# Performance work log

Hardware: AMD Instinct MI355X
Metric: run time of the kernel (lower is better)

The kernel has to match this reference:

```python
import jax, jax.numpy as jnp
import numpy as np

# CSSA config (index=0): H=W=64, strip windows h_spa=64, w_spa=8, heads=4, C=64
B, HW, C, HEADS = 32, 64, 64, 4
HS, WS = 64, 8          # h_spa, w_spa
HD = C // HEADS          # head_dim = 16
WIN = HS * WS            # 512 tokens per window
SCALE = HD ** -0.5


def setup_inputs() -> dict:
    key = jax.random.key(0)
    k1, k2, k3 = jax.random.split(key, 3)
    qkv = jax.random.normal(k1, (3, B, HW * HW, C), dtype=jnp.float32)
    w_conv = jax.random.normal(k2, (C, 1, 3, 3), dtype=jnp.float32) * 0.1
    b_conv = jax.random.normal(k3, (C,), dtype=jnp.float32) * 0.1
    return {"qkv": qkv, "w_conv": w_conv, "b_conv": b_conv}


def _to_img(x):
    # [B, N, C] -> [B, C, H, W]
    return jnp.transpose(x.reshape(B, HW, HW, C), (0, 3, 1, 2))


def _img2window_heads(x):
    img = _to_img(x)
    img = img.reshape(B, C, HW // HS, HS, HW // WS, WS)
    win = jnp.transpose(img, (0, 2, 4, 3, 5, 1)).reshape(-1, WIN, C)
    return jnp.transpose(win.reshape(-1, WIN, HEADS, HD), (0, 2, 1, 3))


def _v_windows(x):
    # [B, N, C] -> [B*nWin, C, h_spa, w_spa] (image-layout windows for conv)
    img = _to_img(x)
    img = img.reshape(B, C, HW // HS, HS, HW // WS, WS)
    return jnp.transpose(img, (0, 2, 4, 1, 3, 5)).reshape(-1, C, HS, WS)


def reference(qkv, w_conv, b_conv):
    q, k, v = qkv[0], qkv[1], qkv[2]
    qh = _img2window_heads(q) * SCALE
    kh = _img2window_heads(k)
    vw = _v_windows(v)                           # [Bw, C, HS, WS]
    # depthwise 3x3 conv LePE
    lepe = jax.lax.conv_general_dilated(
        vw, w_conv, window_strides=(1, 1), padding=((1, 1), (1, 1)),
        feature_group_count=C,
        dimension_numbers=("NCHW", "OIHW", "NCHW")) + b_conv[None, :, None, None]
    Bw = vw.shape[0]
    lepe = jnp.transpose(lepe.reshape(Bw, HEADS, HD, WIN), (0, 1, 3, 2))
    vh = jnp.transpose(vw.reshape(Bw, HEADS, HD, WIN), (0, 1, 3, 2))
    attn = jax.nn.softmax(jnp.einsum("whqd,whkd->whqk", qh, kh), axis=-1)
    x = jnp.einsum("whqk,whkd->whqd", attn, vh) + lepe
    x = jnp.transpose(x, (0, 2, 1, 3)).reshape(Bw, WIN, C)
    # window2spa
    x = x.reshape(B, HW // HS, HW // WS, HS, WS, C)
    x = jnp.transpose(x, (0, 1, 3, 2, 4, 5)).reshape(B, HW * HW, C)
    return x
```

## Files before the change

kernel.cpp:

```cpp
#include <hip/hip_runtime.h>
#include <stdint.h>

#define KSTR 36
#define VSTR 516

typedef __attribute__((ext_vector_type(4))) short          short4v;
typedef __attribute__((ext_vector_type(4))) float          f32x4;
typedef __attribute__((ext_vector_type(4))) unsigned short us4;
typedef __bf16 bf2_t __attribute__((ext_vector_type(2)));

__device__ __forceinline__ float bf2f(unsigned short u) {
    union { unsigned int i; float f; } x; x.i = ((unsigned int)u) << 16; return x.f;
}
__device__ __forceinline__ unsigned int pk2bf(float lo, float hi) {
#if __has_builtin(__builtin_amdgcn_cvt_pk_bf16_f32)
    union { bf2_t v; unsigned int u; } c;
    c.v = __builtin_amdgcn_cvt_pk_bf16_f32(lo, hi);
    return c.u;
#else
    union { float f; unsigned int u; } a, b; a.f = lo; b.f = hi;
    return __builtin_amdgcn_perm(b.u + 0x8000u, a.u + 0x8000u, 0x07060302u);
#endif
}
__device__ __forceinline__ short4v pk4bf(float a, float b, float c, float d) {
    union { short4v s; unsigned int u[2]; } p;
    p.u[0] = pk2bf(a, b);
    p.u[1] = pk2bf(c, d);
    return p.s;
}

__global__ __launch_bounds__(1024, 4)
void CSSA_69355131896243_kernel(const float* __restrict__ qkv,
                                const float* __restrict__ wconv,
                                const float* __restrict__ bconv,
                                float* __restrict__ out)
{
    __shared__ unsigned short Kl[512 * KSTR];
    __shared__ unsigned short Vt[32 * VSTR];
    __shared__ float Wl[288];
    __shared__ float Bl[32];

    const int tid  = threadIdx.x;
    const int wave = tid >> 6, lane = tid & 63, quad = lane >> 4, l15 = lane & 15;

    const int bid = blockIdx.x;
    const int p   = (bid >> 3) & 1;
    const int win = (bid & 7) * 32 + (bid >> 4);
    const int b   = win >> 3, wx = win & 7;
    const int pc  = p * 32;

    const size_t ONE  = (size_t)32 * 4096 * 64;
    const size_t base = ((size_t)b * 4096 + (size_t)wx * 8) * 64;
    const float* gQ = qkv + base;
    const float* gK = qkv + ONE + base;
    const float* gV = qkv + 2 * ONE + base;

    {
        const int c8 = tid & 7;
        const int t0 = tid >> 3;
        #pragma unroll
        for (int r = 0; r < 4; ++r) {
            const int t = r * 128 + t0;
            const size_t goff = (size_t)(t >> 3) * 4096 + (size_t)(t & 7) * 64 + pc + c8 * 4;
            f32x4 kd = *(const f32x4*)(gK + goff);
            f32x4 vd = *(const f32x4*)(gV + goff);
            union { us4 v; unsigned int u[2]; } kb;
            kb.u[0] = pk2bf(kd[0], kd[1]);
            kb.u[1] = pk2bf(kd[2], kd[3]);
            *(us4*)(&Kl[t * KSTR + c8 * 4]) = kb.v;
            const unsigned int v01 = pk2bf(vd[0], vd[1]);
            const unsigned int v23 = pk2bf(vd[2], vd[3]);
            Vt[(c8 * 4 + 0) * VSTR + t] = (unsigned short)(v01 & 0xffffu);
            Vt[(c8 * 4 + 1) * VSTR + t] = (unsigned short)(v01 >> 16);
            Vt[(c8 * 4 + 2) * VSTR + t] = (unsigned short)(v23 & 0xffffu);
            Vt[(c8 * 4 + 3) * VSTR + t] = (unsigned short)(v23 >> 16);
        }
    }
    if (tid < 288) Wl[tid] = wconv[p * 288 + tid];
    if (tid < 32)  Bl[tid] = bconv[pc + tid];

    const float SCL = 0.25f * 1.44269504088896341f;
    const int hl  = (wave & 1) * 16;
    const int hg  = pc + hl;
    const int q0  = (wave >> 1) * 64;
    short4v qf[4];
    #pragma unroll
    for (int t = 0; t < 4; ++t) {
        const int q = q0 + t * 16 + l15;
        f32x4 qv = *(const f32x4*)(gQ + (size_t)(q >> 3) * 4096 + (size_t)(q & 7) * 64 + hg + quad * 4);
        qf[t] = pk4bf(qv[0] * SCL, qv[1] * SCL, qv[2] * SCL, qv[3] * SCL);
    }
    __syncthreads();

    f32x4 acc[4];
    float lp[4];
    #pragma unroll
    for (int t = 0; t < 4; ++t) { acc[t] = (f32x4)0.0f; lp[t] = 0.0f; }

    #pragma unroll 4
    for (int c = 0; c < 32; ++c) {
        const short4v kf = *(const short4v*)(&Kl[(c * 16 + l15) * KSTR + hl + quad * 4]);
        const short4v vf = *(const short4v*)(&Vt[(hl + l15) * VSTR + c * 16 + quad * 4]);
        #pragma unroll
        for (int t = 0; t < 4; ++t) {
            f32x4 s = __builtin_amdgcn_mfma_f32_16x16x16bf16_1k(kf, qf[t], (f32x4)0.0f, 0, 0, 0);
            const float p0 = __builtin_amdgcn_exp2f(s[0]);
            const float p1 = __builtin_amdgcn_exp2f(s[1]);
            const float p2 = __builtin_amdgcn_exp2f(s[2]);
            const float p3 = __builtin_amdgcn_exp2f(s[3]);
            lp[t] += (p0 + p1) + (p2 + p3);
            acc[t] = __builtin_amdgcn_mfma_f32_16x16x16bf16_1k(vf, pk4bf(p0, p1, p2, p3), acc[t], 0, 0, 0);
        }
    }

    float linv[4];
    #pragma unroll
    for (int t = 0; t < 4; ++t) {
        float v = lp[t];
        v += __shfl_xor(v, 16, 64);
        v += __shfl_xor(v, 32, 64);
        linv[t] = __builtin_amdgcn_rcpf(v);
    }

    #pragma unroll
    for (int j = 0; j < 4; ++j) {
        const int dl = hl + quad * 4 + j;
        float w9[9];
        #pragma unroll
        for (int o = 0; o < 9; ++o) w9[o] = Wl[dl * 9 + o];
        const float bs = Bl[dl];
        const unsigned short* vrow = &Vt[dl * VSTR];
        #pragma unroll
        for (int t = 0; t < 4; ++t) {
            const int q = q0 + t * 16 + l15;
            const int y = q >> 3, x = q & 7;
            float lep = bs;
            #pragma unroll
            for (int dy = 0; dy < 3; ++dy) {
                #pragma unroll
                for (int dx = 0; dx < 3; ++dx) {
                    const int yy = y + dy - 1, xx = x + dx - 1;
                    const bool ok = ((unsigned)yy < 64u) && ((unsigned)xx < 8u);
                    const int tt = (q + (dy - 1) * 8 + (dx - 1)) & 511;
                    lep += (ok ? w9[dy * 3 + dx] : 0.0f) * bf2f(vrow[tt]);
                }
            }
            acc[t][j] = acc[t][j] * linv[t] + lep;
        }
    }
    float* gO = out + base;
    #pragma unroll
    for (int t = 0; t < 4; ++t) {
        const int q = q0 + t * 16 + l15;
        *(f32x4*)(gO + (size_t)(q >> 3) * 4096 + (size_t)(q & 7) * 64 + hg + quad * 4) = acc[t];
    }
}

extern "C" void kernel_launch(void* const* d_in, const int* in_sizes, int n_in,
                              void* d_out, int out_size, void* d_ws, size_t ws_size,
                              hipStream_t stream) {
    const float* qkv   = (const float*)d_in[0];
    const float* wconv = (const float*)d_in[1];
    const float* bconv = (const float*)d_in[2];
    float* outp = (float*)d_out;
    hipLaunchKernelGGL(CSSA_69355131896243_kernel, dim3(512), dim3(1024), 0, stream,
                       qkv, wconv, bconv, outp);
}
```

Measured before the change: 214.5 us.

## Pre-swizzle K/V LDS layouts into MFMA fragment order and prefetch fragments

K and V are stored in LDS in a fragment-major layout so each lane's 4-element bf16 MFMA operand is contiguous and chunk blocks are 512 apart, replacing the padded row/transposed layouts. The next chunk's K/V fragments are loaded one iteration ahead to hide LDS latency. Conv weights and bias are now read straight from global into registers instead of staged in LDS, and the LePE loop is restructured to compute neighbour indices once per query. The V stores during staging are scalar 16-bit writes in the new layout, which may bank-conflict, and register pressure rises from the 36 held weights.

```diff
diff --git a/kernel.cpp b/kernel.cpp
--- a/kernel.cpp
+++ b/kernel.cpp
@@ -1,8 +1,6 @@
 #include <hip/hip_runtime.h>
 #include <stdint.h>
 
-#define KSTR 36
-#define VSTR 516
 
 typedef __attribute__((ext_vector_type(4))) short          short4v;
 typedef __attribute__((ext_vector_type(4))) float          f32x4;
@@ -35,10 +33,8 @@
                                 const float* __restrict__ bconv,
                                 float* __restrict__ out)
 {
-    __shared__ unsigned short Kl[512 * KSTR];
-    __shared__ unsigned short Vt[32 * VSTR];
-    __shared__ float Wl[288];
-    __shared__ float Bl[32];
+    __shared__ unsigned short Kl[16384];
+    __shared__ unsigned short Vl[16384];
 
     const int tid  = threadIdx.x;
     const int wave = tid >> 6, lane = tid & 63, quad = lane >> 4, l15 = lane & 15;
@@ -58,6 +54,7 @@
     {
         const int c8 = tid & 7;
         const int t0 = tid >> 3;
+        const int shh = c8 >> 2, dq = c8 & 3;
         #pragma unroll
         for (int r = 0; r < 4; ++r) {
             const int t = r * 128 + t0;
@@ -67,22 +64,22 @@
             union { us4 v; unsigned int u[2]; } kb;
             kb.u[0] = pk2bf(kd[0], kd[1]);
             kb.u[1] = pk2bf(kd[2], kd[3]);
-            *(us4*)(&Kl[t * KSTR + c8 * 4]) = kb.v;
+            const int kidx = (t >> 4) * 512 + shh * 256 + dq * 64 + (t & 15) * 4;
+            *(us4*)(&Kl[kidx]) = kb.v;
             const unsigned int v01 = pk2bf(vd[0], vd[1]);
             const unsigned int v23 = pk2bf(vd[2], vd[3]);
-            Vt[(c8 * 4 + 0) * VSTR + t] = (unsigned short)(v01 & 0xffffu);
-            Vt[(c8 * 4 + 1) * VSTR + t] = (unsigned short)(v01 >> 16);
-            Vt[(c8 * 4 + 2) * VSTR + t] = (unsigned short)(v23 & 0xffffu);
-            Vt[(c8 * 4 + 3) * VSTR + t] = (unsigned short)(v23 >> 16);
+            const int vidx = (t >> 4) * 512 + shh * 256 + ((t >> 2) & 3) * 64 + dq * 16 + (t & 3);
+            Vl[vidx +  0] = (unsigned short)(v01 & 0xffffu);
+            Vl[vidx +  4] = (unsigned short)(v01 >> 16);
+            Vl[vidx +  8] = (unsigned short)(v23 & 0xffffu);
+            Vl[vidx + 12] = (unsigned short)(v23 >> 16);
         }
     }
-    if (tid < 288) Wl[tid] = wconv[p * 288 + tid];
-    if (tid < 32)  Bl[tid] = bconv[pc + tid];
 
     const float SCL = 0.25f * 1.44269504088896341f;
-    const int hl  = (wave & 1) * 16;
-    const int hg  = pc + hl;
-    const int q0  = (wave >> 1) * 64;
+    const int hh = wave & 1;
+    const int hg = pc + hh * 16;
+    const int q0 = (wave >> 1) * 64;
     short4v qf[4];
     #pragma unroll
     for (int t = 0; t < 4; ++t) {
@@ -97,10 +94,14 @@
     #pragma unroll
     for (int t = 0; t < 4; ++t) { acc[t] = (f32x4)0.0f; lp[t] = 0.0f; }
 
+    const int foff = hh * 256 + quad * 64 + l15 * 4;
+    short4v kf = *(const short4v*)(&Kl[foff]);
+    short4v vf = *(const short4v*)(&Vl[foff]);
     #pragma unroll 4
     for (int c = 0; c < 32; ++c) {
-        const short4v kf = *(const short4v*)(&Kl[(c * 16 + l15) * KSTR + hl + quad * 4]);
-        const short4v vf = *(const short4v*)(&Vt[(hl + l15) * VSTR + c * 16 + quad * 4]);
+        const int nx = foff + ((c + 1) & 31) * 512;
+        const short4v kfn = *(const short4v*)(&Kl[nx]);
+        const short4v vfn = *(const short4v*)(&Vl[nx]);
         #pragma unroll
         for (int t = 0; t < 4; ++t) {
             f32x4 s = __builtin_amdgcn_mfma_f32_16x16x16bf16_1k(kf, qf[t], (f32x4)0.0f, 0, 0, 0);
@@ -111,6 +112,7 @@
             lp[t] += (p0 + p1) + (p2 + p3);
             acc[t] = __builtin_amdgcn_mfma_f32_16x16x16bf16_1k(vf, pk4bf(p0, p1, p2, p3), acc[t], 0, 0, 0);
         }
+        kf = kfn; vf = vfn;
     }
 
     float linv[4];
@@ -122,29 +124,39 @@
         linv[t] = __builtin_amdgcn_rcpf(v);
     }
 
+    float w9[4][9], bs4[4];
     #pragma unroll
     for (int j = 0; j < 4; ++j) {
-        const int dl = hl + quad * 4 + j;
-        float w9[9];
+        const int ch = hg + quad * 4 + j;
         #pragma unroll
-        for (int o = 0; o < 9; ++o) w9[o] = Wl[dl * 9 + o];
-        const float bs = Bl[dl];
-        const unsigned short* vrow = &Vt[dl * VSTR];
+        for (int o = 0; o < 9; ++o) w9[j][o] = wconv[ch * 9 + o];
+        bs4[j] = bconv[ch];
+    }
+    #pragma unroll
+    for (int t = 0; t < 4; ++t) {
+        const int q = q0 + t * 16 + l15;
+        const int y = q >> 3, x = l15 & 7;
+        int  pidx[9];
+        bool okm[9];
         #pragma unroll
-        for (int t = 0; t < 4; ++t) {
-            const int q = q0 + t * 16 + l15;
-            const int y = q >> 3, x = q & 7;
-            float lep = bs;
+        for (int dy = 0; dy < 3; ++dy) {
+            const int yy = y + dy - 1;
+            const bool oky = ((unsigned)yy < 64u);
             #pragma unroll
-            for (int dy = 0; dy < 3; ++dy) {
-                #pragma unroll
-                for (int dx = 0; dx < 3; ++dx) {
-                    const int yy = y + dy - 1, xx = x + dx - 1;
-                    const bool ok = ((unsigned)yy < 64u) && ((unsigned)xx < 8u);
-                    const int tt = (q + (dy - 1) * 8 + (dx - 1)) & 511;
-                    lep += (ok ? w9[dy * 3 + dx] : 0.0f) * bf2f(vrow[tt]);
-                }
+            for (int dx = 0; dx < 3; ++dx) {
+                const int o  = dy * 3 + dx;
+                const int xx = x + dx - 1;
+                okm[o] = oky && ((unsigned)xx < 8u);
+                const int tt = (q + (dy - 1) * 8 + (dx - 1)) & 511;
+                pidx[o] = (tt >> 4) * 512 + hh * 256 + ((tt >> 2) & 3) * 64 + quad * 16 + (tt & 3);
             }
+        }
+        #pragma unroll
+        for (int j = 0; j < 4; ++j) {
+            float lep = bs4[j];
+            #pragma unroll
+            for (int o = 0; o < 9; ++o)
+                lep += (okm[o] ? w9[j][o] : 0.0f) * bf2f(Vl[pidx[o] + j * 4]);
             acc[t][j] = acc[t][j] * linv[t] + lep;
         }
     }
```

After: 217.3 us. No clear change (+1.3%).
